# Kernel tuning notes

Hardware: AMD Instinct MI355X
Metric: run time of the kernel (lower is better)

## Reference

```python
import jax, jax.numpy as jnp
import numpy as np

N_NODES = 40000
N_EDGES = 640000
DIM = 128
N_BASIS = 50
N_FILTERS = 128
CUTOFF = 5.0
LOG2 = float(np.log(2.0))
PI = float(np.pi)


def ssp(t):
    # ShiftedSoftplus: softplus(x) - log(2), numerically stable via logaddexp
    return jnp.logaddexp(t, 0.0) - LOG2


def setup_inputs() -> dict:
    key = jax.random.key(0)
    ks = jax.random.split(key, 16)
    u = lambda k, shape, fan_in: jax.random.uniform(k, shape, jnp.float32, -1.0, 1.0) / np.sqrt(fan_in)
    return {
        "x": jax.random.normal(ks[0], (N_NODES, DIM), jnp.float32),
        "r_ij": jax.random.uniform(ks[1], (N_EDGES,), jnp.float32) * CUTOFF,
        "f_ij": jax.random.normal(ks[2], (N_EDGES, N_BASIS), jnp.float32),
        "ind_i": jax.random.randint(ks[3], (N_EDGES,), 0, N_NODES),
        "ind_j": jax.random.randint(ks[4], (N_EDGES,), 0, N_NODES),
        # parameters
        "W_in2f": u(ks[5], (DIM, N_FILTERS), DIM),            # Linear(dim, n_filters, bias=False)
        "W_f1": u(ks[6], (N_BASIS, N_FILTERS), N_BASIS),       # filter_network Linear 1
        "b_f1": u(ks[7], (N_FILTERS,), N_BASIS),
        "W_f2": u(ks[8], (N_FILTERS, N_FILTERS), N_FILTERS),   # filter_network Linear 2
        "b_f2": u(ks[9], (N_FILTERS,), N_FILTERS),
        "W_out": u(ks[10], (N_FILTERS, DIM), N_FILTERS),       # f2out Linear
        "b_out": u(ks[11], (DIM,), N_FILTERS),
        "W_lin": u(ks[12], (DIM, DIM), DIM),                   # final lin
        "b_lin": u(ks[13], (DIM,), DIM),
    }


def reference(x, r_ij, f_ij, ind_i, ind_j,
              W_in2f, W_f1, b_f1, W_f2, b_f2, W_out, b_out, W_lin, b_lin):
    # filter network: Linear -> ShiftedSoftplus -> Linear, on edges: [E, nf]
    W = ssp(f_ij @ W_f1 + b_f1) @ W_f2 + b_f2
    # cosine cutoff: [E]
    C = 0.5 * (jnp.cos(r_ij * (PI / CUTOFF)) + 1.0) * (r_ij < CUTOFF).astype(r_ij.dtype)
    W = W * C[:, None]
    # node embedding -> filters: [N, nf]
    h = x @ W_in2f
    # gather source nodes, modulate by filters: [E, nf]
    msg = h[ind_j] * W
    # scatter-add pool to destination nodes: [N, nf]
    agg = jax.ops.segment_sum(msg, ind_i, num_segments=x.shape[0])
    # f2out: Linear -> ShiftedSoftplus, then final Linear
    v = ssp(agg @ W_out + b_out)
    return v @ W_lin + b_lin
```

## Files before the change

### kernel.cpp

```cpp
#include <hip/hip_runtime.h>
#include <hip/hip_fp16.h>

#define N_NODES_C 40000
#define N_EDGES_C 640000
#define DIM 128
#define NB 50
#define LDA 132
#define BLK 256
#define TROWS 64
#define LOG2_C 0.6931471805599453f
#define PI_OVER_CUT 0.6283185307179586f
#define NSCAN_BLK 157

typedef __attribute__((ext_vector_type(8))) short s8v;
typedef __attribute__((ext_vector_type(4))) float f4v;

#define MFMA_BF16 __builtin_amdgcn_mfma_f32_16x16x32_bf16

#define SEG_IN2F_H 0
#define SEG_IN2F_L 20480
#define SEG_F1_H   40960
#define SEG_F1_L   51200
#define SEG_F2_H   61440
#define SEG_F2_L   81920
#define SEG_OUT_H  102400
#define SEG_OUT_L  122880
#define SEG_LIN_H  143360
#define SEG_LIN_L  163840
#define WSPLIT_USHORTS 184320

__device__ __forceinline__ unsigned short f2bf(float x) {
    unsigned int u = __float_as_uint(x);
    u += 0x7fffu + ((u >> 16) & 1u);
    return (unsigned short)(u >> 16);
}
__device__ __forceinline__ float bf2f(unsigned short h) {
    return __uint_as_float(((unsigned int)h) << 16);
}
__device__ __forceinline__ float ssp_f(float t) {
    float e = __expf(-fabsf(t));
    return fmaxf(t, 0.0f) + __logf(1.0f + e) - LOG2_C;
}
__device__ __forceinline__ void split8t(const float* av, s8v& Ah, s8v& Al) {
#pragma unroll
    for (int j = 0; j < 8; j += 2) {
        unsigned int u0 = __float_as_uint(av[j]);
        unsigned int u1 = __float_as_uint(av[j + 1]);
        float h0 = __uint_as_float(u0 & 0xffff0000u);
        float h1 = __uint_as_float(u1 & 0xffff0000u);
        unsigned int r0 = __float_as_uint(av[j] - h0);
        unsigned int r1 = __float_as_uint(av[j + 1] - h1);
        ((unsigned int*)&Ah)[j >> 1] = __builtin_amdgcn_perm(u1, u0, 0x07060302);
        ((unsigned int*)&Al)[j >> 1] = __builtin_amdgcn_perm(r1, r0, 0x07060302);
    }
}
__device__ __forceinline__ void f2x4_to_split(const float2 v[4], s8v& Ah, s8v& Al) {
    float av[8] = {v[0].x, v[0].y, v[1].x, v[1].y, v[2].x, v[2].y, v[3].x, v[3].y};
    split8t(av, Ah, Al);
}
__device__ __forceinline__ void loadB4(const unsigned short* __restrict__ p, s8v B[4]) {
#pragma unroll
    for (int t = 0; t < 4; ++t) B[t] = *(const s8v*)(p + t * 640);
}
__device__ __forceinline__ void mfma8_half(const s8v B[4], const s8v& A0, const s8v& A1,
                                           f4v acc0[4], f4v acc1[4]) {
#pragma unroll
    for (int t = 0; t < 4; ++t) {
        acc0[t] = MFMA_BF16(A0, B[t], acc0[t], 0, 0, 0);
        acc1[t] = MFMA_BF16(A1, B[t], acc1[t], 0, 0, 0);
    }
}
__device__ __forceinline__ void mfma16_half(const s8v B[4], const s8v& Ah0, const s8v& Al0,
                                            const s8v& Ah1, const s8v& Al1,
                                            f4v acc0[4], f4v acc1[4]) {
#pragma unroll
    for (int t = 0; t < 4; ++t) {
        acc0[t] = MFMA_BF16(Al0, B[t], acc0[t], 0, 0, 0);
        acc0[t] = MFMA_BF16(Ah0, B[t], acc0[t], 0, 0, 0);
        acc1[t] = MFMA_BF16(Al1, B[t], acc1[t], 0, 0, 0);
        acc1[t] = MFMA_BF16(Ah1, B[t], acc1[t], 0, 0, 0);
    }
}
__device__ __forceinline__ void mfma4x2(const unsigned short* __restrict__ bh,
                                        const unsigned short* __restrict__ bl,
                                        const s8v& Ah0, const s8v& Al0,
                                        const s8v& Ah1, const s8v& Al1,
                                        f4v acc0[4], f4v acc1[4]) {
    s8v B[4];
    loadB4(bl, B);
    mfma8_half(B, Ah0, Ah1, acc0, acc1);
    loadB4(bh, B);
    mfma16_half(B, Ah0, Al0, Ah1, Al1, acc0, acc1);
}
__device__ __forceinline__ void init_acc_cols(f4v acc0[4], f4v acc1[4],
                                              const float* __restrict__ b, int colbase, int lr) {
#pragma unroll
    for (int t = 0; t < 4; ++t) {
        float bv = b[colbase + t * 16 + lr];
        acc0[t] = (f4v){bv, bv, bv, bv};
        acc1[t] = (f4v){bv, bv, bv, bv};
    }
}
__device__ __forceinline__ void gemm_lds_ws(const unsigned short* __restrict__ t1h,
                                            const unsigned short* __restrict__ t1l,
                                            int rowA0, int rowA1, int lk,
                                            const unsigned short* __restrict__ bh,
                                            const unsigned short* __restrict__ bl,
                                            f4v acc0[4], f4v acc1[4]) {
    s8v BlA[4], BhA[4], BlB[4], BhB[4];
    loadB4(bl, BlA);
    loadB4(bh, BhA);
#define KC_STEP(K, BL, BH, BLN, BHN, LOADNEXT)                                 \
    {                                                                          \
        s8v Ah0 = *(const s8v*)&t1h[rowA0 * 136 + (K) * 32 + lk * 8];          \
        s8v Al0 = *(const s8v*)&t1l[rowA0 * 136 + (K) * 32 + lk * 8];          \
        s8v Ah1 = *(const s8v*)&t1h[rowA1 * 136 + (K) * 32 + lk * 8];          \
        s8v Al1 = *(const s8v*)&t1l[rowA1 * 136 + (K) * 32 + lk * 8];          \
        mfma8_half(BL, Ah0, Ah1, acc0, acc1);                                  \
        if (LOADNEXT) loadB4(bl + ((K) + 1) * 5120, BLN);                      \
        mfma16_half(BH, Ah0, Al0, Ah1, Al1, acc0, acc1);                       \
        if (LOADNEXT) loadB4(bh + ((K) + 1) * 5120, BHN);                      \
    }
    KC_STEP(0, BlA, BhA, BlB, BhB, true)
    KC_STEP(1, BlB, BhB, BlA, BhA, true)
    KC_STEP(2, BlA, BhA, BlB, BhB, true)
    KC_STEP(3, BlB, BhB, BlA, BhA, false)
#undef KC_STEP
}
__device__ __forceinline__ void store_t1_ssp(const f4v acc0[4], const f4v acc1[4],
                                             unsigned short* __restrict__ t1h,
                                             unsigned short* __restrict__ t1l,
                                             int rpair, int colbase, int lk, int lr) {
#pragma unroll
    for (int t = 0; t < 4; ++t)
#pragma unroll
        for (int r = 0; r < 4; ++r) {
            int col = colbase + t * 16 + lr;
            float v = ssp_f(acc0[t][r]);
            unsigned int u = __float_as_uint(v);
            float hf = __uint_as_float(u & 0xffff0000u);
            int idx = (rpair * 32 + lk * 4 + r) * 136 + col;
            t1h[idx] = (unsigned short)(u >> 16);
            t1l[idx] = (unsigned short)(__float_as_uint(v - hf) >> 16);
            v = ssp_f(acc1[t][r]);
            u = __float_as_uint(v);
            hf = __uint_as_float(u & 0xffff0000u);
            idx = (rpair * 32 + 16 + lk * 4 + r) * 136 + col;
            t1h[idx] = (unsigned short)(u >> 16);
            t1l[idx] = (unsigned short)(__float_as_uint(v - hf) >> 16);
        }
}

__global__ __launch_bounds__(BLK) void split5_kernel(const float* __restrict__ Wa,
                                                     const float* __restrict__ Wb,
                                                     const float* __restrict__ Wc,
                                                     const float* __restrict__ Wd,
                                                     const float* __restrict__ We,
                                                     unsigned short* __restrict__ Ws) {
    int i = blockIdx.x * BLK + threadIdx.x;
    if (i >= 18 * 4096) return;
    int chunk = i >> 12, r = i & 4095, k = r & 31, col = r >> 5;
    const float* W; int Kr, ck, hb, lb;
    if (chunk < 4)       { W = Wa; Kr = 128; ck = chunk;      hb = SEG_IN2F_H; lb = SEG_IN2F_L; }
    else if (chunk < 6)  { W = Wb; Kr = 50;  ck = chunk - 4;  hb = SEG_F1_H;   lb = SEG_F1_L; }
    else if (chunk < 10) { W = Wc; Kr = 128; ck = chunk - 6;  hb = SEG_F2_H;   lb = SEG_F2_L; }
    else if (chunk < 14) { W = Wd; Kr = 128; ck = chunk - 10; hb = SEG_OUT_H;  lb = SEG_OUT_L; }
    else                 { W = We; Kr = 128; ck = chunk - 14; hb = SEG_LIN_H;  lb = SEG_LIN_L; }
    int krow = ck * 32 + k;
    float v = (krow < Kr) ? W[(size_t)krow * DIM + col] : 0.f;
    unsigned short h16 = f2bf(v);
    int o = ck * 5120 + col * 40 + k;
    Ws[hb + o] = h16;
    Ws[lb + o] = f2bf(v - bf2f(h16));
}

__global__ __launch_bounds__(BLK, 4) void node_in2f_mfma(const float* __restrict__ x,
                                                         const unsigned short* __restrict__ Ws,
                                                         float* __restrict__ h) {
    const int tid = threadIdx.x;
    const int w = tid >> 6, l = tid & 63, lr = l & 15, lk = l >> 4;
    const int rpair = w & 1, colbase = (w >> 1) * 64;
    const int n0 = blockIdx.x * TROWS;
    const int rowA0 = rpair * 32 + lr, rowA1 = rowA0 + 16;
    const float* xr0 = x + (size_t)(n0 + rowA0) * DIM;
    const float* xr1 = x + (size_t)(n0 + rowA1) * DIM;

    f4v acc0[4], acc1[4];
#pragma unroll
    for (int t = 0; t < 4; ++t) {
        acc0[t] = (f4v){0.f, 0.f, 0.f, 0.f};
        acc1[t] = (f4v){0.f, 0.f, 0.f, 0.f};
    }
#pragma unroll
    for (int kc = 0; kc < 4; ++kc) {
        const float* ap0 = xr0 + kc * 32 + lk * 8;
        const float* ap1 = xr1 + kc * 32 + lk * 8;
        float4 a0 = *(const float4*)ap0, a1 = *(const float4*)(ap0 + 4);
        float4 b0 = *(const float4*)ap1, b1 = *(const float4*)(ap1 + 4);
        float av0[8] = {a0.x, a0.y, a0.z, a0.w, a1.x, a1.y, a1.z, a1.w};
        float av1[8] = {b0.x, b0.y, b0.z, b0.w, b1.x, b1.y, b1.z, b1.w};
        s8v Ah0, Al0, Ah1, Al1;
        split8t(av0, Ah0, Al0);
        split8t(av1, Ah1, Al1);
        const int bo = kc * 5120 + (colbase + lr) * 40 + lk * 8;
        mfma4x2(Ws + SEG_IN2F_H + bo, Ws + SEG_IN2F_L + bo, Ah0, Al0, Ah1, Al1, acc0, acc1);
    }
#pragma unroll
    for (int t = 0; t < 4; ++t)
#pragma unroll
        for (int r = 0; r < 4; ++r) {
            int col = colbase + t * 16 + lr;
            h[(size_t)(n0 + rpair * 32 + lk * 4 + r) * DIM + col] = acc0[t][r];
            h[(size_t)(n0 + rpair * 32 + 16 + lk * 4 + r) * DIM + col] = acc1[t][r];
        }
}

__global__ __launch_bounds__(BLK) void hist_kernel(const int* __restrict__ ind_i,
                                                   int* __restrict__ cnt) {
    int e = blockIdx.x * BLK + threadIdx.x;
    if (e < N_EDGES_C) atomicAdd(&cnt[ind_i[e]], 1);
}

__global__ __launch_bounds__(BLK) void scan1_kernel(const int* __restrict__ cnt,
                                                    int* __restrict__ excl,
                                                    int* __restrict__ bsum) {
    __shared__ int s[BLK];
    const int tid = threadIdx.x;
    const int idx = blockIdx.x * BLK + tid;
    int v = (idx < N_NODES_C) ? cnt[idx] : 0;
    s[tid] = v;
    __syncthreads();
    for (int off = 1; off < BLK; off <<= 1) {
        int t = (tid >= off) ? s[tid - off] : 0;
        __syncthreads();
        s[tid] += t;
        __syncthreads();
    }
    if (idx < N_NODES_C) excl[idx] = s[tid] - v;
    if (tid == BLK - 1) bsum[blockIdx.x] = s[tid];
}

__global__ __launch_bounds__(BLK) void scan2_kernel(int* __restrict__ bsum) {
    __shared__ int s[BLK];
    const int tid = threadIdx.x;
    int v = (tid < NSCAN_BLK) ? bsum[tid] : 0;
    s[tid] = v;
    __syncthreads();
    for (int off = 1; off < BLK; off <<= 1) {
        int t = (tid >= off) ? s[tid - off] : 0;
        __syncthreads();
        s[tid] += t;
        __syncthreads();
    }
    if (tid < NSCAN_BLK) bsum[tid] = s[tid] - v;
}

__global__ __launch_bounds__(BLK) void scan3_kernel(int* __restrict__ start,
                                                    int* __restrict__ cursor,
                                                    const int* __restrict__ bsum) {
    const int idx = blockIdx.x * BLK + threadIdx.x;
    if (idx < N_NODES_C) {
        int v = start[idx] + bsum[blockIdx.x];
        start[idx] = v;
        cursor[idx] = v;
    }
}

__global__ __launch_bounds__(BLK) void place_kernel(const int* __restrict__ ind_i,
                                                    int* __restrict__ cursor,
                                                    int* __restrict__ pos) {
    int e = blockIdx.x * BLK + threadIdx.x;
    if (e < N_EDGES_C) {
        int slot = atomicAdd(&cursor[ind_i[e]], 1);
        pos[e] = slot;
    }
}

__global__ __launch_bounds__(BLK, 4) void edge_kernel_mfma(const float* __restrict__ f_ij,
                                                           const float* __restrict__ r_ij,
                                                           const int* __restrict__ ind_j,
                                                           const int* __restrict__ pos,
                                                           const unsigned short* __restrict__ Ws,
                                                           const float* __restrict__ b_f1,
                                                           const float* __restrict__ b_f2,
                                                           const float* __restrict__ h,
                                                           __half* __restrict__ msg) {
    __shared__ __align__(16) char smem[34816];
    unsigned short* t1h = (unsigned short*)smem;
    unsigned short* t1l = t1h + 64 * 136;
    float* tf = (float*)smem;

    const int tid = threadIdx.x;
    const int w = tid >> 6, l = tid & 63, lr = l & 15, lk = l >> 4;
    const int rt = tid >> 4, ct = tid & 15;
    const int rpair = w & 1, colbase = (w >> 1) * 64;
    const int e0 = blockIdx.x * TROWS;
    const int rowA0 = rpair * 32 + lr, rowA1 = rowA0 + 16;
    const int boff = (colbase + lr) * 40 + lk * 8;

    const float* fr0 = f_ij + (size_t)(e0 + rowA0) * NB;
    const float* fr1 = f_ij + (size_t)(e0 + rowA1) * NB;
    float2 fv[2][2][4];
#pragma unroll
    for (int kc = 0; kc < 2; ++kc)
#pragma unroll
        for (int ii = 0; ii < 4; ++ii) {
            int k = kc * 32 + lk * 8 + ii * 2;
            fv[kc][0][ii] = (k < NB) ? *(const float2*)(fr0 + k) : make_float2(0.f, 0.f);
            fv[kc][1][ii] = (k < NB) ? *(const float2*)(fr1 + k) : make_float2(0.f, 0.f);
        }

    f4v acc0[4], acc1[4];
    init_acc_cols(acc0, acc1, b_f1, colbase, lr);
    const unsigned short* f1h = Ws + SEG_F1_H + boff;
    const unsigned short* f1l = Ws + SEG_F1_L + boff;
    {
        s8v BlA[4], BhA[4], BlB[4], BhB[4];
        loadB4(f1l, BlA);
        loadB4(f1h, BhA);
        {
            s8v Ah0, Al0, Ah1, Al1;
            f2x4_to_split(fv[0][0], Ah0, Al0);
            f2x4_to_split(fv[0][1], Ah1, Al1);
            mfma8_half(BlA, Ah0, Ah1, acc0, acc1);
            loadB4(f1l + 5120, BlB);
            mfma16_half(BhA, Ah0, Al0, Ah1, Al1, acc0, acc1);
            loadB4(f1h + 5120, BhB);
        }
        {
            s8v Ah0, Al0, Ah1, Al1;
            f2x4_to_split(fv[1][0], Ah0, Al0);
            f2x4_to_split(fv[1][1], Ah1, Al1);
            mfma8_half(BlB, Ah0, Ah1, acc0, acc1);
            mfma16_half(BhB, Ah0, Al0, Ah1, Al1, acc0, acc1);
        }
    }
    store_t1_ssp(acc0, acc1, t1h, t1l, rpair, colbase, lk, lr);
    float rr4[4]; int nj4[4], ps4[4];
#pragma unroll
    for (int i = 0; i < 4; ++i) {
        int e = e0 + rt * 4 + i;
        rr4[i] = r_ij[e];
        nj4[i] = ind_j[e];
        ps4[i] = pos[e];
    }
    __syncthreads();

    init_acc_cols(acc0, acc1, b_f2, colbase, lr);
    gemm_lds_ws(t1h, t1l, rowA0, rowA1, lk,
                Ws + SEG_F2_H + boff, Ws + SEG_F2_L + boff, acc0, acc1);

    float4 hv[4][2];
#pragma unroll
    for (int i = 0; i < 4; ++i) {
        const float* hp = &h[(size_t)nj4[i] * DIM + ct * 8];
        hv[i][0] = *(const float4*)hp;
        hv[i][1] = *(const float4*)(hp + 4);
    }
    __syncthreads();
#pragma unroll
    for (int t = 0; t < 4; ++t)
#pragma unroll
        for (int r = 0; r < 4; ++r) {
            int col = colbase + t * 16 + lr;
            tf[(rpair * 32 + lk * 4 + r) * LDA + col] = acc0[t][r];
            tf[(rpair * 32 + 16 + lk * 4 + r) * LDA + col] = acc1[t][r];
        }
    __syncthreads();

#pragma unroll
    for (int i = 0; i < 4; ++i) {
        float C = (rr4[i] < 5.0f) ? (0.5f * __cosf(rr4[i] * PI_OVER_CUT) + 0.5f) : 0.0f;
        const float* ep = &tf[(rt * 4 + i) * LDA + ct * 8];
        float4 a0 = *(const float4*)ep, a1 = *(const float4*)(ep + 4);
        float4 h0 = hv[i][0], h1 = hv[i][1];
        __half2 o0 = __floats2half2_rn(h0.x * a0.x * C, h0.y * a0.y * C);
        __half2 o1 = __floats2half2_rn(h0.z * a0.z * C, h0.w * a0.w * C);
        __half2 o2 = __floats2half2_rn(h1.x * a1.x * C, h1.y * a1.y * C);
        __half2 o3 = __floats2half2_rn(h1.z * a1.z * C, h1.w * a1.w * C);
        __half* mp = &msg[(size_t)ps4[i] * DIM + ct * 8];
        *(uint4*)mp = make_uint4(*(unsigned int*)&o0, *(unsigned int*)&o1,
                                 *(unsigned int*)&o2, *(unsigned int*)&o3);
    }
}

__global__ __launch_bounds__(BLK, 4) void node_out_fused(const __half* __restrict__ msg,
                                                         const int* __restrict__ start,
                                                         const int* __restrict__ cnt,
                                                         const unsigned short* __restrict__ Ws,
                                                         const float* __restrict__ b_out,
                                                         const float* __restrict__ b_lin,
                                                         float* __restrict__ out) {
    __shared__ __align__(16) char smem[34816];
    unsigned short* t1h = (unsigned short*)smem;
    unsigned short* t1l = t1h + 64 * 136;

    const int tid = threadIdx.x;
    const int w = tid >> 6, l = tid & 63, lr = l & 15, lk = l >> 4;
    const int rpair = w & 1, colbase = (w >> 1) * 64;
    const int n0 = blockIdx.x * TROWS;
    const int rowA0 = rpair * 32 + lr, rowA1 = rowA0 + 16;
    const int boff = (colbase + lr) * 40 + lk * 8;

    const int q = tid >> 4, l16 = tid & 15;
#pragma unroll
    for (int i = 0; i < 4; ++i) {
        int nrow = q * 4 + i;
        int node = n0 + nrow;
        int s = start[node];
        int d = cnt[node];
        float a[8] = {0.f, 0.f, 0.f, 0.f, 0.f, 0.f, 0.f, 0.f};
        const __half* bp = msg + (size_t)s * DIM + l16 * 8;
        for (int k = 0; k < d; ++k) {
            uint4 v = *(const uint4*)(bp + (size_t)k * DIM);
            const __half2* hp2 = (const __half2*)&v;
#pragma unroll
            for (int j = 0; j < 4; ++j) {
                float2 f = __half22float2(hp2[j]);
                a[j * 2] += f.x;
                a[j * 2 + 1] += f.y;
            }
        }
        s8v Ah, Al;
        split8t(a, Ah, Al);
        *(s8v*)&t1h[nrow * 136 + l16 * 8] = Ah;
        *(s8v*)&t1l[nrow * 136 + l16 * 8] = Al;
    }
    __syncthreads();

    f4v acc0[4], acc1[4];
    init_acc_cols(acc0, acc1, b_out, colbase, lr);
    gemm_lds_ws(t1h, t1l, rowA0, rowA1, lk,
                Ws + SEG_OUT_H + boff, Ws + SEG_OUT_L + boff, acc0, acc1);
    __syncthreads();
    store_t1_ssp(acc0, acc1, t1h, t1l, rpair, colbase, lk, lr);
    __syncthreads();

    init_acc_cols(acc0, acc1, b_lin, colbase, lr);
    gemm_lds_ws(t1h, t1l, rowA0, rowA1, lk,
                Ws + SEG_LIN_H + boff, Ws + SEG_LIN_L + boff, acc0, acc1);
#pragma unroll
    for (int t = 0; t < 4; ++t)
#pragma unroll
        for (int r = 0; r < 4; ++r) {
            int col = colbase + t * 16 + lr;
            out[(size_t)(n0 + rpair * 32 + lk * 4 + r) * DIM + col] = acc0[t][r];
            out[(size_t)(n0 + rpair * 32 + 16 + lk * 4 + r) * DIM + col] = acc1[t][r];
        }
}

__device__ __forceinline__ void stage_chunk(const float* __restrict__ B, int k0, int rows,
                                            float* __restrict__ Bc, int tid) {
    const int n4 = rows * (DIM / 4);
    const float4* Bg = (const float4*)B + (size_t)k0 * (DIM / 4);
    float4* Bc4 = (float4*)Bc;
    for (int i = tid; i < n4; i += BLK) Bc4[i] = Bg[i];
}

__device__ __forceinline__ void init_acc_bias(float acc[4][8], const float* __restrict__ b, int ct) {
    float4 bb0 = *(const float4*)&b[ct * 8];
    float4 bb1 = *(const float4*)&b[ct * 8 + 4];
#pragma unroll
    for (int i = 0; i < 4; ++i) {
        acc[i][0] = bb0.x; acc[i][1] = bb0.y; acc[i][2] = bb0.z; acc[i][3] = bb0.w;
        acc[i][4] = bb1.x; acc[i][5] = bb1.y; acc[i][6] = bb1.z; acc[i][7] = bb1.w;
    }
}

template <int KPAD>
__device__ __forceinline__ void gemm_tile(const float* __restrict__ A_lds, int lda,
                                          const float* __restrict__ Bglob,
                                          float* __restrict__ Bc,
                                          float acc[4][8], int rt, int ct, int tid) {
    for (int k0 = 0; k0 < KPAD; k0 += 32) {
        __syncthreads();
        stage_chunk(Bglob, k0, 32, Bc, tid);
        __syncthreads();
#pragma unroll 2
        for (int k4 = 0; k4 < 8; ++k4) {
            float4 av[4];
#pragma unroll
            for (int i = 0; i < 4; ++i)
                av[i] = *(const float4*)&A_lds[(rt * 4 + i) * lda + k0 + k4 * 4];
#pragma unroll
            for (int kk = 0; kk < 4; ++kk) {
                const float* bp = &Bc[(k4 * 4 + kk) * DIM + ct * 8];
                float4 b0 = *(const float4*)bp;
                float4 b1 = *(const float4*)(bp + 4);
#pragma unroll
                for (int i = 0; i < 4; ++i) {
                    float a = ((const float*)&av[i])[kk];
                    acc[i][0] = fmaf(a, b0.x, acc[i][0]);
                    acc[i][1] = fmaf(a, b0.y, acc[i][1]);
                    acc[i][2] = fmaf(a, b0.z, acc[i][2]);
                    acc[i][3] = fmaf(a, b0.w, acc[i][3]);
                    acc[i][4] = fmaf(a, b1.x, acc[i][4]);
                    acc[i][5] = fmaf(a, b1.y, acc[i][5]);
                    acc[i][6] = fmaf(a, b1.z, acc[i][6]);
                    acc[i][7] = fmaf(a, b1.w, acc[i][7]);
                }
            }
        }
    }
}

template <int NK2>
__device__ __forceinline__ void gemm1_direct(const float* const (&frow)[4], int k2base,
                                             const float* __restrict__ Bc,
                                             float acc[4][8], int ct) {
#pragma unroll 4
    for (int k2 = 0; k2 < NK2; ++k2) {
        float2 a2[4];
#pragma unroll
        for (int i = 0; i < 4; ++i)
            a2[i] = *(const float2*)(frow[i] + (k2base + k2) * 2);
#pragma unroll
        for (int kk = 0; kk < 2; ++kk) {
            const float* bp = &Bc[(k2 * 2 + kk) * DIM + ct * 8];
            float4 b0 = *(const float4*)bp;
            float4 b1 = *(const float4*)(bp + 4);
#pragma unroll
            for (int i = 0; i < 4; ++i) {
                float a = kk ? a2[i].y : a2[i].x;
                acc[i][0] = fmaf(a, b0.x, acc[i][0]);
                acc[i][1] = fmaf(a, b0.y, acc[i][1]);
                acc[i][2] = fmaf(a, b0.z, acc[i][2]);
                acc[i][3] = fmaf(a, b0.w, acc[i][3]);
                acc[i][4] = fmaf(a, b1.x, acc[i][4]);
                acc[i][5] = fmaf(a, b1.y, acc[i][5]);
                acc[i][6] = fmaf(a, b1.z, acc[i][6]);
                acc[i][7] = fmaf(a, b1.w, acc[i][7]);
            }
        }
    }
}

__global__ __launch_bounds__(BLK) void node_in2f_fb(const float* __restrict__ x,
                                                    const float* __restrict__ W,
                                                    float* __restrict__ h) {
    __shared__ float At[TROWS * LDA];
    __shared__ float Bc[32 * DIM];
    const int tid = threadIdx.x;
    const int rt = tid >> 4, ct = tid & 15;
    const int n0 = blockIdx.x * TROWS;
    for (int i = tid; i < TROWS * (DIM / 4); i += BLK) {
        int row = i >> 5, c4 = i & 31;
        *(float4*)&At[row * LDA + c4 * 4] = *(const float4*)&x[(size_t)(n0 + row) * DIM + c4 * 4];
    }
    float acc[4][8];
#pragma unroll
    for (int i = 0; i < 4; ++i)
#pragma unroll
        for (int j = 0; j < 8; ++j) acc[i][j] = 0.f;
    gemm_tile<DIM>(At, LDA, W, Bc, acc, rt, ct, tid);
#pragma unroll
    for (int i = 0; i < 4; ++i) {
        float* hp = &h[(size_t)(n0 + rt * 4 + i) * DIM + ct * 8];
        *(float4*)hp = make_float4(acc[i][0], acc[i][1], acc[i][2], acc[i][3]);
        *(float4*)(hp + 4) = make_float4(acc[i][4], acc[i][5], acc[i][6], acc[i][7]);
    }
}

__global__ __launch_bounds__(BLK) void node_out_fb(const float* __restrict__ agg,
                                                   const float* __restrict__ W_out,
                                                   const float* __restrict__ b_out,
                                                   const float* __restrict__ W_lin,
                                                   const float* __restrict__ b_lin,
                                                   float* __restrict__ out) {
    __shared__ float At[TROWS * LDA];
    __shared__ float Bc[32 * DIM];
    const int tid = threadIdx.x;
    const int rt = tid >> 4, ct = tid & 15;
    const int n0 = blockIdx.x * TROWS;
    for (int i = tid; i < TROWS * (DIM / 4); i += BLK) {
        int row = i >> 5, c4 = i & 31;
        *(float4*)&At[row * LDA + c4 * 4] = *(const float4*)&agg[(size_t)(n0 + row) * DIM + c4 * 4];
    }
    float acc[4][8];
    init_acc_bias(acc, b_out, ct);
    gemm_tile<DIM>(At, LDA, W_out, Bc, acc, rt, ct, tid);
    __syncthreads();
#pragma unroll
    for (int i = 0; i < 4; ++i) {
        float* tp = &At[(rt * 4 + i) * LDA + ct * 8];
        *(float4*)tp = make_float4(ssp_f(acc[i][0]), ssp_f(acc[i][1]),
                                   ssp_f(acc[i][2]), ssp_f(acc[i][3]));
        *(float4*)(tp + 4) = make_float4(ssp_f(acc[i][4]), ssp_f(acc[i][5]),
                                         ssp_f(acc[i][6]), ssp_f(acc[i][7]));
    }
    init_acc_bias(acc, b_lin, ct);
    gemm_tile<DIM>(At, LDA, W_lin, Bc, acc, rt, ct, tid);
#pragma unroll
    for (int i = 0; i < 4; ++i) {
        float* op = &out[(size_t)(n0 + rt * 4 + i) * DIM + ct * 8];
        *(float4*)op = make_float4(acc[i][0], acc[i][1], acc[i][2], acc[i][3]);
        *(float4*)(op + 4) = make_float4(acc[i][4], acc[i][5], acc[i][6], acc[i][7]);
    }
}

__global__ __launch_bounds__(BLK) void edge_kernel_atomic(const float* __restrict__ f_ij,
                                                          const float* __restrict__ r_ij,
                                                          const int* __restrict__ ind_i,
                                                          const int* __restrict__ ind_j,
                                                          const float* __restrict__ W_f1,
                                                          const float* __restrict__ b_f1,
                                                          const float* __restrict__ W_f2,
                                                          const float* __restrict__ b_f2,
                                                          const float* __restrict__ h,
                                                          float* __restrict__ agg) {
    __shared__ float t1[TROWS * LDA];
    __shared__ float Bc[32 * DIM];
    const int tid = threadIdx.x;
    const int rt = tid >> 4, ct = tid & 15;
    const int e0 = blockIdx.x * TROWS;
    const float* frow[4];
#pragma unroll
    for (int i = 0; i < 4; ++i) frow[i] = f_ij + (size_t)(e0 + rt * 4 + i) * NB;
    float acc[4][8];
    init_acc_bias(acc, b_f1, ct);
    stage_chunk(W_f1, 0, 32, Bc, tid);
    __syncthreads();
    gemm1_direct<16>(frow, 0, Bc, acc, ct);
    __syncthreads();
    stage_chunk(W_f1, 32, 18, Bc, tid);
    __syncthreads();
    gemm1_direct<9>(frow, 16, Bc, acc, ct);
#pragma unroll
    for (int i = 0; i < 4; ++i) {
        float* tp = &t1[(rt * 4 + i) * LDA + ct * 8];
        *(float4*)tp = make_float4(ssp_f(acc[i][0]), ssp_f(acc[i][1]),
                                   ssp_f(acc[i][2]), ssp_f(acc[i][3]));
        *(float4*)(tp + 4) = make_float4(ssp_f(acc[i][4]), ssp_f(acc[i][5]),
                                         ssp_f(acc[i][6]), ssp_f(acc[i][7]));
    }
    init_acc_bias(acc, b_f2, ct);
    gemm_tile<DIM>(t1, LDA, W_f2, Bc, acc, rt, ct, tid);
#pragma unroll
    for (int i = 0; i < 4; ++i) {
        int e = e0 + rt * 4 + i;
        float r = r_ij[e];
        float C = (r < 5.0f) ? 0.5f * (cosf(r * PI_OVER_CUT) + 1.0f) : 0.0f;
        int nj = ind_j[e];
        int ni = ind_i[e];
        const float* hp = &h[(size_t)nj * DIM + ct * 8];
        float4 h0 = *(const float4*)hp;
        float4 h1 = *(const float4*)(hp + 4);
        float* ap = &agg[(size_t)ni * DIM + ct * 8];
        atomicAdd(ap + 0, h0.x * acc[i][0] * C);
        atomicAdd(ap + 1, h0.y * acc[i][1] * C);
        atomicAdd(ap + 2, h0.z * acc[i][2] * C);
        atomicAdd(ap + 3, h0.w * acc[i][3] * C);
        atomicAdd(ap + 4, h1.x * acc[i][4] * C);
        atomicAdd(ap + 5, h1.y * acc[i][5] * C);
        atomicAdd(ap + 6, h1.z * acc[i][6] * C);
        atomicAdd(ap + 7, h1.w * acc[i][7] * C);
    }
}

extern "C" void kernel_launch(void* const* d_in, const int* in_sizes, int n_in,
                              void* d_out, int out_size, void* d_ws, size_t ws_size,
                              hipStream_t stream) {
    const float* x      = (const float*)d_in[0];
    const float* r_ij   = (const float*)d_in[1];
    const float* f_ij   = (const float*)d_in[2];
    const int*   ind_i  = (const int*)d_in[3];
    const int*   ind_j  = (const int*)d_in[4];
    const float* W_in2f = (const float*)d_in[5];
    const float* W_f1   = (const float*)d_in[6];
    const float* b_f1   = (const float*)d_in[7];
    const float* W_f2   = (const float*)d_in[8];
    const float* b_f2   = (const float*)d_in[9];
    const float* W_out  = (const float*)d_in[10];
    const float* b_out  = (const float*)d_in[11];
    const float* W_lin  = (const float*)d_in[12];
    const float* b_lin  = (const float*)d_in[13];
    float* out = (float*)d_out;

    char* ws = (char*)d_ws;
    size_t off = 0;
    auto alloc = [&](size_t bytes) {
        char* p = ws + off;
        off = (off + bytes + 511) & ~(size_t)511;
        return p;
    };
    unsigned short* Wsplit = (unsigned short*)alloc(WSPLIT_USHORTS * sizeof(unsigned short));
    float*  h      = (float*)alloc((size_t)N_NODES_C * DIM * sizeof(float));
    __half* msg    = (__half*)alloc((size_t)N_EDGES_C * DIM * sizeof(__half));
    int*    pos    = (int*)alloc((size_t)N_EDGES_C * sizeof(int));
    int*    cnt    = (int*)alloc((size_t)N_NODES_C * sizeof(int));
    int*    startA = (int*)alloc((size_t)N_NODES_C * sizeof(int));
    int*    cursor = (int*)alloc((size_t)N_NODES_C * sizeof(int));
    int*    bsum   = (int*)alloc((size_t)NSCAN_BLK * sizeof(int));
    const bool have_ws = (off <= ws_size);

    if (have_ws) {
        split5_kernel<<<(18 * 4096 + BLK - 1) / BLK, BLK, 0, stream>>>(
            W_in2f, W_f1, W_f2, W_out, W_lin, Wsplit);

        node_in2f_mfma<<<N_NODES_C / TROWS, BLK, 0, stream>>>(x, Wsplit, h);

        hipMemsetAsync(cnt, 0, (size_t)N_NODES_C * sizeof(int), stream);
        hist_kernel<<<(N_EDGES_C + BLK - 1) / BLK, BLK, 0, stream>>>(ind_i, cnt);
        scan1_kernel<<<NSCAN_BLK, BLK, 0, stream>>>(cnt, startA, bsum);
        scan2_kernel<<<1, BLK, 0, stream>>>(bsum);
        scan3_kernel<<<NSCAN_BLK, BLK, 0, stream>>>(startA, cursor, bsum);
        place_kernel<<<(N_EDGES_C + BLK - 1) / BLK, BLK, 0, stream>>>(ind_i, cursor, pos);

        edge_kernel_mfma<<<N_EDGES_C / TROWS, BLK, 0, stream>>>(
            f_ij, r_ij, ind_j, pos, Wsplit, b_f1, b_f2, h, msg);

        node_out_fused<<<N_NODES_C / TROWS, BLK, 0, stream>>>(
            msg, startA, cnt, Wsplit, b_out, b_lin, out);
    } else {
        float* h2   = (float*)d_ws;
        float* agg2 = h2 + (size_t)N_NODES_C * DIM;
        node_in2f_fb<<<N_NODES_C / TROWS, BLK, 0, stream>>>(x, W_in2f, h2);
        hipMemsetAsync(agg2, 0, (size_t)N_NODES_C * DIM * sizeof(float), stream);
        edge_kernel_atomic<<<N_EDGES_C / TROWS, BLK, 0, stream>>>(
            f_ij, r_ij, ind_i, ind_j, W_f1, b_f1, W_f2, b_f2, h2, agg2);
        node_out_fb<<<N_NODES_C / TROWS, BLK, 0, stream>>>(agg2, W_out, b_out, W_lin, b_lin, out);
    }
}
```

Measured before the change: 298.4 us.

## Halve edge kernel LDS and registers to raise occupancy to eight blocks

The edge kernel now stores the first-layer activations as a single bf16 copy instead of a hi/lo split, and stores the filter output tile as fp16 instead of fp32. This halves shared memory to 17 KB and lets the launch bound request 8 blocks per CU. Register use also drops because the double-buffered B prefetch and early gathers of h, r, ind_j and pos are removed. In exchange the second GEMM loses the lo part of its A operand, which lowers precision, and the loads lose their latency-hiding prefetch.

```diff
diff --git a/kernel.cpp b/kernel.cpp
--- a/kernel.cpp
+++ b/kernel.cpp
@@ -107,25 +107,18 @@
                                             const unsigned short* __restrict__ bh,
                                             const unsigned short* __restrict__ bl,
                                             f4v acc0[4], f4v acc1[4]) {
-    s8v BlA[4], BhA[4], BlB[4], BhB[4];
-    loadB4(bl, BlA);
-    loadB4(bh, BhA);
-#define KC_STEP(K, BL, BH, BLN, BHN, LOADNEXT)                                 \
-    {                                                                          \
-        s8v Ah0 = *(const s8v*)&t1h[rowA0 * 136 + (K) * 32 + lk * 8];          \
-        s8v Al0 = *(const s8v*)&t1l[rowA0 * 136 + (K) * 32 + lk * 8];          \
-        s8v Ah1 = *(const s8v*)&t1h[rowA1 * 136 + (K) * 32 + lk * 8];          \
-        s8v Al1 = *(const s8v*)&t1l[rowA1 * 136 + (K) * 32 + lk * 8];          \
-        mfma8_half(BL, Ah0, Ah1, acc0, acc1);                                  \
-        if (LOADNEXT) loadB4(bl + ((K) + 1) * 5120, BLN);                      \
-        mfma16_half(BH, Ah0, Al0, Ah1, Al1, acc0, acc1);                       \
-        if (LOADNEXT) loadB4(bh + ((K) + 1) * 5120, BHN);                      \
-    }
-    KC_STEP(0, BlA, BhA, BlB, BhB, true)
-    KC_STEP(1, BlB, BhB, BlA, BhA, true)
-    KC_STEP(2, BlA, BhA, BlB, BhB, true)
-    KC_STEP(3, BlB, BhB, BlA, BhA, false)
-#undef KC_STEP
+#pragma unroll
+    for (int kc = 0; kc < 4; ++kc) {
+        s8v Ah0 = *(const s8v*)&t1h[rowA0 * 136 + kc * 32 + lk * 8];
+        s8v Al0 = *(const s8v*)&t1l[rowA0 * 136 + kc * 32 + lk * 8];
+        s8v Ah1 = *(const s8v*)&t1h[rowA1 * 136 + kc * 32 + lk * 8];
+        s8v Al1 = *(const s8v*)&t1l[rowA1 * 136 + kc * 32 + lk * 8];
+        s8v B[4];
+        loadB4(bl + kc * 5120, B);
+        mfma8_half(B, Ah0, Ah1, acc0, acc1);
+        loadB4(bh + kc * 5120, B);
+        mfma16_half(B, Ah0, Al0, Ah1, Al1, acc0, acc1);
+    }
 }
 __device__ __forceinline__ void store_t1_ssp(const f4v acc0[4], const f4v acc1[4],
                                              unsigned short* __restrict__ t1h,
@@ -276,7 +269,7 @@
     }
 }
 
-__global__ __launch_bounds__(BLK, 4) void edge_kernel_mfma(const float* __restrict__ f_ij,
+__global__ __launch_bounds__(BLK, 8) void edge_kernel_mfma(const float* __restrict__ f_ij,
                                                            const float* __restrict__ r_ij,
                                                            const int* __restrict__ ind_j,
                                                            const int* __restrict__ pos,
@@ -285,10 +278,9 @@
                                                            const float* __restrict__ b_f2,
                                                            const float* __restrict__ h,
                                                            __half* __restrict__ msg) {
-    __shared__ __align__(16) char smem[34816];
-    unsigned short* t1h = (unsigned short*)smem;
-    unsigned short* t1l = t1h + 64 * 136;
-    float* tf = (float*)smem;
+    __shared__ __align__(16) char smem[17408];
+    unsigned short* t1b = (unsigned short*)smem;
+    __half* tfh = (__half*)smem;
 
     const int tid = threadIdx.x;
     const int w = tid >> 6, l = tid & 63, lr = l & 15, lk = l >> 4;
@@ -298,87 +290,82 @@
     const int rowA0 = rpair * 32 + lr, rowA1 = rowA0 + 16;
     const int boff = (colbase + lr) * 40 + lk * 8;
 
+    f4v acc0[4], acc1[4];
+    init_acc_cols(acc0, acc1, b_f1, colbase, lr);
     const float* fr0 = f_ij + (size_t)(e0 + rowA0) * NB;
     const float* fr1 = f_ij + (size_t)(e0 + rowA1) * NB;
-    float2 fv[2][2][4];
-#pragma unroll
-    for (int kc = 0; kc < 2; ++kc)
+    const unsigned short* f1h = Ws + SEG_F1_H + boff;
+    const unsigned short* f1l = Ws + SEG_F1_L + boff;
+#pragma unroll
+    for (int kc = 0; kc < 2; ++kc) {
+        float2 v0[4], v1[4];
 #pragma unroll
         for (int ii = 0; ii < 4; ++ii) {
             int k = kc * 32 + lk * 8 + ii * 2;
-            fv[kc][0][ii] = (k < NB) ? *(const float2*)(fr0 + k) : make_float2(0.f, 0.f);
-            fv[kc][1][ii] = (k < NB) ? *(const float2*)(fr1 + k) : make_float2(0.f, 0.f);
-        }
-
-    f4v acc0[4], acc1[4];
-    init_acc_cols(acc0, acc1, b_f1, colbase, lr);
-    const unsigned short* f1h = Ws + SEG_F1_H + boff;
-    const unsigned short* f1l = Ws + SEG_F1_L + boff;
-    {
-        s8v BlA[4], BhA[4], BlB[4], BhB[4];
-        loadB4(f1l, BlA);
-        loadB4(f1h, BhA);
-        {
-            s8v Ah0, Al0, Ah1, Al1;
-            f2x4_to_split(fv[0][0], Ah0, Al0);
-            f2x4_to_split(fv[0][1], Ah1, Al1);
-            mfma8_half(BlA, Ah0, Ah1, acc0, acc1);
-            loadB4(f1l + 5120, BlB);
-            mfma16_half(BhA, Ah0, Al0, Ah1, Al1, acc0, acc1);
-            loadB4(f1h + 5120, BhB);
-        }
-        {
-            s8v Ah0, Al0, Ah1, Al1;
-            f2x4_to_split(fv[1][0], Ah0, Al0);
-            f2x4_to_split(fv[1][1], Ah1, Al1);
-            mfma8_half(BlB, Ah0, Ah1, acc0, acc1);
-            mfma16_half(BhB, Ah0, Al0, Ah1, Al1, acc0, acc1);
-        }
-    }
-    store_t1_ssp(acc0, acc1, t1h, t1l, rpair, colbase, lk, lr);
-    float rr4[4]; int nj4[4], ps4[4];
+            v0[ii] = (k < NB) ? *(const float2*)(fr0 + k) : make_float2(0.f, 0.f);
+            v1[ii] = (k < NB) ? *(const float2*)(fr1 + k) : make_float2(0.f, 0.f);
+        }
+        s8v Ah0, Al0, Ah1, Al1;
+        f2x4_to_split(v0, Ah0, Al0);
+        f2x4_to_split(v1, Ah1, Al1);
+        s8v B[4];
+        loadB4(f1l + kc * 5120, B);
+        mfma8_half(B, Ah0, Ah1, acc0, acc1);
+        loadB4(f1h + kc * 5120, B);
+        mfma16_half(B, Ah0, Al0, Ah1, Al1, acc0, acc1);
+    }
+#pragma unroll
+    for (int t = 0; t < 4; ++t)
+#pragma unroll
+        for (int r = 0; r < 4; ++r) {
+            int col = colbase + t * 16 + lr;
+            t1b[(rpair * 32 + lk * 4 + r) * 136 + col] = f2bf(ssp_f(acc0[t][r]));
+            t1b[(rpair * 32 + 16 + lk * 4 + r) * 136 + col] = f2bf(ssp_f(acc1[t][r]));
+        }
+    __syncthreads();
+
+    init_acc_cols(acc0, acc1, b_f2, colbase, lr);
+    const unsigned short* f2h = Ws + SEG_F2_H + boff;
+    const unsigned short* f2l = Ws + SEG_F2_L + boff;
+#pragma unroll
+    for (int kc = 0; kc < 4; ++kc) {
+        s8v Ab0 = *(const s8v*)&t1b[rowA0 * 136 + kc * 32 + lk * 8];
+        s8v Ab1 = *(const s8v*)&t1b[rowA1 * 136 + kc * 32 + lk * 8];
+        s8v B[4];
+        loadB4(f2l + kc * 5120, B);
+        mfma8_half(B, Ab0, Ab1, acc0, acc1);
+        loadB4(f2h + kc * 5120, B);
+        mfma8_half(B, Ab0, Ab1, acc0, acc1);
+    }
+    __syncthreads();
+#pragma unroll
+    for (int t = 0; t < 4; ++t)
+#pragma unroll
+        for (int r = 0; r < 4; ++r) {
+            int col = colbase + t * 16 + lr;
+            tfh[(rpair * 32 + lk * 4 + r) * 136 + col] = __float2half_rn(acc0[t][r]);
+            tfh[(rpair * 32 + 16 + lk * 4 + r) * 136 + col] = __float2half_rn(acc1[t][r]);
+        }
+    __syncthreads();
+
 #pragma unroll
     for (int i = 0; i < 4; ++i) {
         int e = e0 + rt * 4 + i;
-        rr4[i] = r_ij[e];
-        nj4[i] = ind_j[e];
-        ps4[i] = pos[e];
-    }
-    __syncthreads();
-
-    init_acc_cols(acc0, acc1, b_f2, colbase, lr);
-    gemm_lds_ws(t1h, t1l, rowA0, rowA1, lk,
-                Ws + SEG_F2_H + boff, Ws + SEG_F2_L + boff, acc0, acc1);
-
-    float4 hv[4][2];
-#pragma unroll
-    for (int i = 0; i < 4; ++i) {
-        const float* hp = &h[(size_t)nj4[i] * DIM + ct * 8];
-        hv[i][0] = *(const float4*)hp;
-        hv[i][1] = *(const float4*)(hp + 4);
-    }
-    __syncthreads();
-#pragma unroll
-    for (int t = 0; t < 4; ++t)
-#pragma unroll
-        for (int r = 0; r < 4; ++r) {
-            int col = colbase + t * 16 + lr;
-            tf[(rpair * 32 + lk * 4 + r) * LDA + col] = acc0[t][r];
-            tf[(rpair * 32 + 16 + lk * 4 + r) * LDA + col] = acc1[t][r];
-        }
-    __syncthreads();
-
-#pragma unroll
-    for (int i = 0; i < 4; ++i) {
-        float C = (rr4[i] < 5.0f) ? (0.5f * __cosf(rr4[i] * PI_OVER_CUT) + 0.5f) : 0.0f;
-        const float* ep = &tf[(rt * 4 + i) * LDA + ct * 8];
-        float4 a0 = *(const float4*)ep, a1 = *(const float4*)(ep + 4);
-        float4 h0 = hv[i][0], h1 = hv[i][1];
-        __half2 o0 = __floats2half2_rn(h0.x * a0.x * C, h0.y * a0.y * C);
-        __half2 o1 = __floats2half2_rn(h0.z * a0.z * C, h0.w * a0.w * C);
-        __half2 o2 = __floats2half2_rn(h1.x * a1.x * C, h1.y * a1.y * C);
-        __half2 o3 = __floats2half2_rn(h1.z * a1.z * C, h1.w * a1.w * C);
-        __half* mp = &msg[(size_t)ps4[i] * DIM + ct * 8];
+        float rr = r_ij[e];
+        float C = (rr < 5.0f) ? (0.5f * __cosf(rr * PI_OVER_CUT) + 0.5f) : 0.0f;
+        int nj = ind_j[e];
+        const __half* ep = &tfh[(rt * 4 + i) * 136 + ct * 8];
+        uint4 av = *(const uint4*)ep;
+        const __half2* ah2 = (const __half2*)&av;
+        const float* hp = &h[(size_t)nj * DIM + ct * 8];
+        float4 h0 = *(const float4*)hp, h1 = *(const float4*)(hp + 4);
+        float2 a01 = __half22float2(ah2[0]), a23 = __half22float2(ah2[1]);
+        float2 a45 = __half22float2(ah2[2]), a67 = __half22float2(ah2[3]);
+        __half2 o0 = __floats2half2_rn(h0.x * a01.x * C, h0.y * a01.y * C);
+        __half2 o1 = __floats2half2_rn(h0.z * a23.x * C, h0.w * a23.y * C);
+        __half2 o2 = __floats2half2_rn(h1.x * a45.x * C, h1.y * a45.y * C);
+        __half2 o3 = __floats2half2_rn(h1.z * a67.x * C, h1.w * a67.y * C);
+        __half* mp = &msg[(size_t)pos[e] * DIM + ct * 8];
         *(uint4*)mp = make_uint4(*(unsigned int*)&o0, *(unsigned int*)&o1,
                                  *(unsigned int*)&o2, *(unsigned int*)&o3);
     }
```

Result: slower. 544.1 us (+82.3%).
